# Performance work log

Measured on AMD Instinct MI355X. Metric: run time of the kernel, lower is better.

The kernel has to match this reference:

```python
import jax, jax.numpy as jnp
import numpy as np

WS = 7       # window size
SHIFT = 3    # shift size (ws//2)
NH = 16      # num heads
DIM = 512    # channels
HH = 112
WW = 112
HIDDEN = int(DIM * 4.0)
EPS = 1e-5


def _rel_index():
    # Swin relative position index, [N, N] ints into the bias table
    coords = np.stack(np.meshgrid(np.arange(WS), np.arange(WS), indexing='ij')).reshape(2, -1)
    rel = coords[:, :, None] - coords[:, None, :]
    rel = rel.transpose(1, 2, 0) + (WS - 1)
    rel[:, :, 0] *= 2 * WS - 1
    return rel.sum(-1)


def _attn_mask():
    # shifted-window mask on HH x WW (already multiples of WS) -> [nW, N, N] with 0 / -1e9
    img = np.zeros((HH, WW), np.int32)
    cnt = 0
    sl = (slice(0, -WS), slice(-WS, -SHIFT), slice(-SHIFT, None))
    for h in sl:
        for w in sl:
            img[h, w] = cnt
            cnt += 1
    win = img.reshape(HH // WS, WS, WW // WS, WS).transpose(0, 2, 1, 3).reshape(-1, WS * WS)
    diff = win[:, None, :] - win[:, :, None]
    return np.where(diff == 0, 0.0, -1e9).astype(np.float32)


def setup_inputs() -> dict:
    key = jax.random.key(0)
    ks = jax.random.split(key, 8)
    s = 0.02
    return {
        'x': jax.random.normal(ks[0], (DIM, HH, WW), jnp.float32),
        'norm1_w': jnp.ones((DIM,), jnp.float32),
        'norm1_b': jnp.zeros((DIM,), jnp.float32),
        'qkv_w': jax.random.normal(ks[1], (3 * DIM, DIM), jnp.float32) * s,
        'qkv_b': jnp.zeros((3 * DIM,), jnp.float32),
        'proj_w': jax.random.normal(ks[2], (DIM, DIM), jnp.float32) * s,
        'proj_b': jnp.zeros((DIM,), jnp.float32),
        'rpb_table': jax.random.normal(ks[3], ((2 * WS - 1) ** 2, NH), jnp.float32) * s,
        'norm2_w': jnp.ones((DIM,), jnp.float32),
        'norm2_b': jnp.zeros((DIM,), jnp.float32),
        'fc1_w': jax.random.normal(ks[4], (HIDDEN, DIM), jnp.float32) * s,
        'fc1_b': jnp.zeros((HIDDEN,), jnp.float32),
        'fc2_w': jax.random.normal(ks[5], (DIM, HIDDEN), jnp.float32) * s,
        'fc2_b': jnp.zeros((DIM,), jnp.float32),
    }


def _ln(x_hwc, w, b):
    m = x_hwc.mean(-1, keepdims=True)
    v = x_hwc.var(-1, keepdims=True)
    return (x_hwc - m) / jnp.sqrt(v + EPS) * w + b


def reference(x, norm1_w, norm1_b, qkv_w, qkv_b, proj_w, proj_b, rpb_table,
              norm2_w, norm2_b, fc1_w, fc1_b, fc2_w, fc2_b):
    C, H, W = x.shape
    ws = WS
    N = ws * ws
    hd = C // NH
    scale = 1.0 / np.sqrt(hd).astype(np.float32)

    x_hwc = jnp.moveaxis(x, 0, -1)                       # [H,W,C]
    xn = _ln(x_hwc, norm1_w, norm1_b)
    xs = jnp.roll(xn, (-SHIFT, -SHIFT), (0, 1))          # cyclic shift
    # window partition -> [nW, N, C]
    xw = xs.reshape(H // ws, ws, W // ws, ws, C).transpose(0, 2, 1, 3, 4).reshape(-1, N, C)

    qkv = xw @ qkv_w.T + qkv_b                            # [nW,N,3C]
    q, k, v = jnp.split(qkv, 3, -1)
    heads = lambda t: t.reshape(-1, N, NH, hd).transpose(0, 2, 1, 3)  # [nW,H,N,hd]
    q, k, v = heads(q), heads(k), heads(v)

    attn = jnp.einsum('whnd,whmd->whnm', q * scale, k)    # [nW,H,N,N]
    idx = jnp.asarray(_rel_index().reshape(-1))
    bias = rpb_table[idx].reshape(N, N, NH).transpose(2, 0, 1)  # [H,N,N]
    mask = jnp.asarray(_attn_mask())                       # [nW,N,N]
    attn = attn + bias[None] + mask[:, None]
    attn = jax.nn.softmax(attn, -1)

    out = jnp.einsum('whnm,whmd->whnd', attn, v).transpose(0, 2, 1, 3).reshape(-1, N, C)
    out = out @ proj_w.T + proj_b
    # window unpartition + reverse shift
    out = out.reshape(H // ws, W // ws, ws, ws, C).transpose(0, 2, 1, 3, 4).reshape(H, W, C)
    out = jnp.roll(out, (SHIFT, SHIFT), (0, 1))

    x1 = x_hwc + out                                       # residual (DropPath rate 0)
    x2 = _ln(x1, norm2_w, norm2_b)
    h = jax.nn.gelu(x2.reshape(-1, C) @ fc1_w.T + fc1_b)
    m = (h @ fc2_w.T + fc2_b).reshape(H, W, C)
    y = x1 + m
    return jnp.moveaxis(y, -1, 0)                          # back to [C,H,W]
```

## Files before the change

### kernel.cpp

```cpp
#include <hip/hip_runtime.h>

#define NPIX 12544
#define CDIM 512
#define QKVN 1536
#define HIDDEN 2048

typedef unsigned short u16;
typedef unsigned int u32;

typedef short bf16x8 __attribute__((ext_vector_type(8)));
typedef float f32x4 __attribute__((ext_vector_type(4)));

static __device__ __forceinline__ u16 f2bf(float f) {
  u32 u = __float_as_uint(f);
  return (u16)((u + 0x7fffu + ((u >> 16) & 1u)) >> 16);
}
static __device__ __forceinline__ u32 pack2(float a, float b) {
  return (u32)f2bf(a) | ((u32)f2bf(b) << 16);
}
static __device__ __forceinline__ u32 packtrunc2(float lo, float hi) {
  return __builtin_amdgcn_perm(__float_as_uint(hi), __float_as_uint(lo), 0x07060302u);
}
static __device__ __forceinline__ void async_ld16(const void* g, void* l) {
  __builtin_amdgcn_global_load_lds((__attribute__((address_space(1))) void*)g,
                                   (__attribute__((address_space(3))) void*)l, 16, 0, 0);
}

__global__ __launch_bounds__(256) void convert_weights(
    const float* __restrict__ qw, const float* __restrict__ pw,
    const float* __restrict__ w1, const float* __restrict__ w2,
    u16* __restrict__ Wq, u16* __restrict__ Wp, u16* __restrict__ W1o, u16* __restrict__ W2o) {
  const int b = blockIdx.x;
  const float* src; u16* dst; long off;
  if (b < 768)       { src = qw; dst = Wq;  off = (long)b * 1024; }
  else if (b < 1024) { src = pw; dst = Wp;  off = (long)(b - 768) * 1024; }
  else if (b < 2048) { src = w1; dst = W1o; off = (long)(b - 1024) * 1024; }
  else               { src = w2; dst = W2o; off = (long)(b - 2048) * 1024; }
  const long i = off / 4 + threadIdx.x;
  const float4 v = ((const float4*)src)[i];
  ushort4 u;
  u.x = f2bf(v.x); u.y = f2bf(v.y); u.z = f2bf(v.z); u.w = f2bf(v.w);
  ((ushort4*)dst)[i] = u;
}

__global__ __launch_bounds__(256) void ln1_partial(const float* __restrict__ x,
                                                   float* __restrict__ psum, float* __restrict__ pssq) {
  const int p = blockIdx.x * 256 + threadIdx.x;
  const int c0 = blockIdx.y * 32;
  float s = 0.f, ss = 0.f;
#pragma unroll
  for (int c = 0; c < 32; c++) {
    const float v = x[(long)(c0 + c) * NPIX + p];
    s += v; ss += v * v;
  }
  psum[blockIdx.y * NPIX + p] = s;
  pssq[blockIdx.y * NPIX + p] = ss;
}

__global__ __launch_bounds__(256) void ln1_stats(const float* __restrict__ psum, const float* __restrict__ pssq,
                                                 float* __restrict__ mean, float* __restrict__ rstd) {
  const int p = blockIdx.x * 256 + threadIdx.x;
  float s = 0.f, ss = 0.f;
#pragma unroll
  for (int ch = 0; ch < 16; ch++) { s += psum[ch * NPIX + p]; ss += pssq[ch * NPIX + p]; }
  const float m = s * (1.f / 512.f);
  const float v = ss * (1.f / 512.f) - m * m;
  mean[p] = m;
  rstd[p] = rsqrtf(v + 1e-5f);
}

__global__ __launch_bounds__(256) void ln1_shift_part(const float* __restrict__ x,
    const float* __restrict__ mean, const float* __restrict__ rstd,
    const float* __restrict__ gw, const float* __restrict__ gb, u16* __restrict__ xw) {
  __shared__ float tile[32][65];
  const int p0 = blockIdx.x * 64;
  const int c0 = blockIdx.y * 32;
  const int t = threadIdx.x;
  {
    const int pl = t & 63;
    const int cl0 = t >> 6;
#pragma unroll
    for (int r = 0; r < 8; r++) {
      const int cl = r * 4 + cl0;
      tile[cl][pl] = x[(long)(c0 + cl) * NPIX + p0 + pl];
    }
  }
  __syncthreads();
  const int cl = t & 31;
  const int g = t >> 5;
  const float wc = gw[c0 + cl];
  const float bc = gb[c0 + cl];
#pragma unroll
  for (int pass = 0; pass < 8; pass++) {
    const int pl = pass * 8 + g;
    const int p = p0 + pl;
    const int h = p / 112;
    const int w = p - h * 112;
    int hs = h + 109; if (hs >= 112) hs -= 112;
    int ws2 = w + 109; if (ws2 >= 112) ws2 -= 112;
    const int hq = hs / 7, wq = ws2 / 7;
    const int tok = (hq * 16 + wq) * 49 + (hs - hq * 7) * 7 + (ws2 - wq * 7);
    const float val = (tile[cl][pl] - mean[p]) * rstd[p] * wc + bc;
    xw[(long)tok * 512 + c0 + cl] = f2bf(val);
  }
}

template<bool OUT_BF16, bool DO_GELU, bool REMAP>
__global__ __launch_bounds__(256, 3) void gemm_bt(
    const u16* __restrict__ A, const u16* __restrict__ B,
    const float* __restrict__ bias, void* __restrict__ out,
    const int N, const int K) {
  __shared__ __align__(16) u16 Asm[128 * 32];
  __shared__ __align__(16) u16 Bsm[128 * 32];
  const int M0 = blockIdx.x << 7;
  const int N0 = blockIdx.y << 7;
  const int t = threadIdx.x;
  const int wave = t >> 6;
  const int lane = t & 63;
  const int l15 = lane & 15;
  const int quad = lane >> 4;
  const int wm = wave & 1;
  const int wn = wave >> 1;
  const int swz = (l15 >> 1) & 3;

  f32x4 acc[4][4] = {};

  for (int k0 = 0; k0 < K; k0 += 32) {
#pragma unroll
    for (int i = 0; i < 2; i++) {
      const int flatbase = i * 256 + wave * 64;
      const int FL = flatbase + lane;
      const int row = FL >> 2;
      const int chunk = (FL & 3) ^ ((row >> 1) & 3);
      async_ld16(A + (long)(M0 + row) * K + k0 + chunk * 8, &Asm[flatbase * 8]);
      async_ld16(B + (long)(N0 + row) * K + k0 + chunk * 8, &Bsm[flatbase * 8]);
    }
    __syncthreads();
    bf16x8 af[4], bfr[4];
#pragma unroll
    for (int im = 0; im < 4; im++)
      af[im] = *(const bf16x8*)&Asm[(wm * 64 + im * 16 + l15) * 32 + (quad ^ swz) * 8];
#pragma unroll
    for (int in = 0; in < 4; in++)
      bfr[in] = *(const bf16x8*)&Bsm[(wn * 64 + in * 16 + l15) * 32 + (quad ^ swz) * 8];
#pragma unroll
    for (int im = 0; im < 4; im++)
#pragma unroll
      for (int in = 0; in < 4; in++)
        acc[im][in] = __builtin_amdgcn_mfma_f32_16x16x32_bf16(bfr[in], af[im], acc[im][in], 0, 0, 0);
    __syncthreads();
  }

#pragma unroll
  for (int im = 0; im < 4; im++) {
    const int row = M0 + wm * 64 + im * 16 + l15;
    long orow = row;
    if (REMAP) {
      const int win = row / 49;
      const int nn = row - win * 49;
      const int nq = nn / 7;
      const int hs = (win >> 4) * 7 + nq;
      const int wsx = (win & 15) * 7 + (nn - nq * 7);
      int h = hs + 3; if (h >= 112) h -= 112;
      int w = wsx + 3; if (w >= 112) w -= 112;
      orow = h * 112 + w;
    }
#pragma unroll
    for (int in = 0; in < 4; in++) {
      const int col0 = N0 + wn * 64 + in * 16 + quad * 4;
      const float4 bv = *(const float4*)(bias + col0);
      float v[4];
#pragma unroll
      for (int r = 0; r < 4; r++) {
        float vv = acc[im][in][r] + ((const float*)&bv)[r];
        if (DO_GELU) {
          const float z2 = 1.5957691216f * (vv + 0.044715f * vv * vv * vv);
          vv = vv / (1.0f + __expf(-z2));
        }
        v[r] = vv;
      }
      if (OUT_BF16) {
        uint2 u;
        u.x = pack2(v[0], v[1]);
        u.y = pack2(v[2], v[3]);
        *(uint2*)((u16*)out + orow * (long)N + col0) = u;
      } else {
        float4 f; f.x = v[0]; f.y = v[1]; f.z = v[2]; f.w = v[3];
        *(float4*)((float*)out + orow * (long)N + col0) = f;
      }
    }
  }
}

__global__ __launch_bounds__(256) void build_biasT(const float* __restrict__ rpb, float* __restrict__ biasT) {
  const int cls = blockIdx.x >> 4;
  const int head = blockIdx.x & 15;
  for (int e = threadIdx.x; e < 4096; e += 256) {
    const int j = e >> 6;
    const int i = e & 63;
    float v;
    if (j >= 49) v = -1e9f;
    else if (i >= 49) v = 0.f;
    else {
      const int ri = i / 7, ci = i - (i / 7) * 7;
      const int rj = j / 7, cj = j - (j / 7) * 7;
      v = rpb[((ri - rj + 6) * 13 + (ci - cj + 6)) * 16 + head];
      const int lhi = (cls & 2) ? (ri < 4 ? 1 : 2) : 0;
      const int lwi = (cls & 1) ? (ci < 4 ? 1 : 2) : 0;
      const int lhj = (cls & 2) ? (rj < 4 ? 1 : 2) : 0;
      const int lwj = (cls & 1) ? (cj < 4 ? 1 : 2) : 0;
      if (lhi * 3 + lwi != lhj * 3 + lwj) v = -1e9f;
    }
    biasT[(long)blockIdx.x * 4096 + e] = v;
  }
}

__global__ __launch_bounds__(256, 3) void attn_mfma(
    const u16* __restrict__ qkv, const float* __restrict__ biasT, u16* __restrict__ out) {
  __shared__ __align__(16) u16 slds[24576];
  const int t = threadIdx.x;
  const int wave = t >> 6;
  const int lane = t & 63;
  const int l15 = lane & 15;
  const int quad = lane >> 4;
  const int win = blockIdx.x >> 2;
  const int head = (blockIdx.x & 3) * 4 + wave;
  const int cls = (((win >> 4) == 15) ? 2 : 0) | (((win & 15) == 15) ? 1 : 0);

  u16* Qb  = slds + wave * 6144;
  u16* Kb  = Qb + 2048;
  u16* Vtb = Qb + 4096;
  u16* Pb  = Qb;

  const int rrow = lane >> 2;
  const int chunk = (lane & 3) ^ ((lane >> 3) & 3);
  uint4 vv[4];
#pragma unroll
  for (int it = 0; it < 4; it++) {
    const int row = it * 16 + rrow;
    const int jc = row < 49 ? row : 48;
    const long gbase = (long)(win * 49 + jc) * 1536 + head * 32 + chunk * 8;
    async_ld16(qkv + gbase,       Qb + it * 512 + lane * 8);
    async_ld16(qkv + gbase + 512, Kb + it * 512 + lane * 8);
    vv[it] = *(const uint4*)(qkv + gbase + 1024);
  }
  __syncthreads();

#pragma unroll
  for (int it = 0; it < 4; it++) {
    const int row = it * 16 + rrow;
    const u32* w = (const u32*)&vv[it];
#pragma unroll
    for (int tt = 0; tt < 8; tt++) {
      const int d = chunk * 8 + tt;
      const u16 val = (tt & 1) ? (u16)(w[tt >> 1] >> 16) : (u16)(w[tt >> 1] & 0xffffu);
      Vtb[d * 64 + (row ^ (((d >> 2) & 3) << 4))] = val;
    }
  }

  const int fswz = (l15 >> 1) & 3;
  bf16x8 kfrag[4], qfrag[4];
#pragma unroll
  for (int jm = 0; jm < 4; jm++)
    kfrag[jm] = *(const bf16x8*)(Kb + (jm * 16 + l15) * 32 + (quad ^ fswz) * 8);
#pragma unroll
  for (int in = 0; in < 4; in++)
    qfrag[in] = *(const bf16x8*)(Qb + (in * 16 + l15) * 32 + (quad ^ fswz) * 8);
  f32x4 sacc[4][4] = {};
#pragma unroll
  for (int jm = 0; jm < 4; jm++)
#pragma unroll
    for (int in = 0; in < 4; in++)
      sacc[jm][in] = __builtin_amdgcn_mfma_f32_16x16x32_bf16(kfrag[jm], qfrag[in], sacc[jm][in], 0, 0, 0);

  const float* bT = biasT + (long)(cls * 16 + head) * 4096;
  const float sc = 0.17677669529663687f;
#pragma unroll
  for (int jm = 0; jm < 4; jm++) {
    const float* bp = bT + (jm * 16 + quad * 4) * 64 + l15;
#pragma unroll
    for (int in = 0; in < 4; in++)
#pragma unroll
      for (int r = 0; r < 4; r++)
        sacc[jm][in][r] = sacc[jm][in][r] * sc + bp[r * 64 + in * 16];
  }
  float linv[4];
#pragma unroll
  for (int in = 0; in < 4; in++) {
    float m = -1e30f;
#pragma unroll
    for (int jm = 0; jm < 4; jm++)
#pragma unroll
      for (int r = 0; r < 4; r++) m = fmaxf(m, sacc[jm][in][r]);
    m = fmaxf(m, __shfl_xor(m, 16));
    m = fmaxf(m, __shfl_xor(m, 32));
    float s = 0.f;
#pragma unroll
    for (int jm = 0; jm < 4; jm++)
#pragma unroll
      for (int r = 0; r < 4; r++) {
        const float e = __expf(sacc[jm][in][r] - m);
        sacc[jm][in][r] = e; s += e;
      }
    s += __shfl_xor(s, 16);
    s += __shfl_xor(s, 32);
    linv[in] = __builtin_amdgcn_rcpf(s);
  }

#pragma unroll
  for (int in = 0; in < 4; in++) {
    const int i = in * 16 + l15;
    const int rot = (l15 & 3) << 4;
#pragma unroll
    for (int jm = 0; jm < 4; jm++) {
      const u32 lo = packtrunc2(sacc[jm][in][0], sacc[jm][in][1]);
      const u32 hi = packtrunc2(sacc[jm][in][2], sacc[jm][in][3]);
      uint2 u; u.x = lo; u.y = hi;
      *(uint2*)(Pb + i * 64 + ((jm * 16 + quad * 4) ^ rot)) = u;
    }
  }

  f32x4 oacc[2][4] = {};
#pragma unroll
  for (int ks = 0; ks < 2; ks++) {
    bf16x8 vtf[2], pf[4];
#pragma unroll
    for (int dm = 0; dm < 2; dm++)
      vtf[dm] = *(const bf16x8*)(Vtb + (dm * 16 + l15) * 64 + ((ks * 32 + quad * 8) ^ ((l15 >> 2) << 4)));
#pragma unroll
    for (int in = 0; in < 4; in++)
      pf[in] = *(const bf16x8*)(Pb + (in * 16 + l15) * 64 + ((ks * 32 + quad * 8) ^ ((l15 & 3) << 4)));
#pragma unroll
    for (int dm = 0; dm < 2; dm++)
#pragma unroll
      for (int in = 0; in < 4; in++)
        oacc[dm][in] = __builtin_amdgcn_mfma_f32_16x16x32_bf16(vtf[dm], pf[in], oacc[dm][in], 0, 0, 0);
  }

#pragma unroll
  for (int in = 0; in < 4; in++) {
    const int i = in * 16 + l15;
    if (i < 49) {
      const float inv = linv[in];
      const long base = (long)(win * 49 + i) * 512 + head * 32 + quad * 4;
#pragma unroll
      for (int dm = 0; dm < 2; dm++) {
        const float v0 = oacc[dm][in][0] * inv, v1 = oacc[dm][in][1] * inv;
        const float v2 = oacc[dm][in][2] * inv, v3 = oacc[dm][in][3] * inv;
        uint2 u; u.x = packtrunc2(v0, v1); u.y = packtrunc2(v2, v3);
        *(uint2*)(out + base + dm * 16) = u;
      }
    }
  }
}

__global__ __launch_bounds__(256) void resid_kernel(const float* __restrict__ x,
    const float* __restrict__ proj, float* __restrict__ x1) {
  __shared__ float tile[32][65];
  const int p0 = blockIdx.x * 64;
  const int c0 = blockIdx.y * 32;
  const int t = threadIdx.x;
  {
    const int pl = t & 63;
    const int cl0 = t >> 6;
#pragma unroll
    for (int r = 0; r < 8; r++) {
      const int cl = r * 4 + cl0;
      tile[cl][pl] = x[(long)(c0 + cl) * NPIX + p0 + pl];
    }
  }
  __syncthreads();
  const int cl = t & 31;
  const int g = t >> 5;
#pragma unroll
  for (int pass = 0; pass < 8; pass++) {
    const int pl = pass * 8 + g;
    const long idx = (long)(p0 + pl) * 512 + c0 + cl;
    x1[idx] = tile[cl][pl] + proj[idx];
  }
}

__global__ __launch_bounds__(256) void ln2_apply(const float* __restrict__ x1,
    const float* __restrict__ gw, const float* __restrict__ gb, u16* __restrict__ x2) {
  const int wave = threadIdx.x >> 6;
  const int lane = threadIdx.x & 63;
  const int p = blockIdx.x * 4 + wave;
  const float4* row = (const float4*)(x1 + (long)p * 512);
  const float4 a = row[lane * 2];
  const float4 b = row[lane * 2 + 1];
  float s = a.x + a.y + a.z + a.w + b.x + b.y + b.z + b.w;
  float ss = a.x * a.x + a.y * a.y + a.z * a.z + a.w * a.w
           + b.x * b.x + b.y * b.y + b.z * b.z + b.w * b.w;
#pragma unroll
  for (int o = 32; o > 0; o >>= 1) { s += __shfl_xor(s, o); ss += __shfl_xor(ss, o); }
  const float m = s * (1.f / 512.f);
  const float var = ss * (1.f / 512.f) - m * m;
  const float rs = rsqrtf(var + 1e-5f);
  const float4 w0 = ((const float4*)gw)[lane * 2];
  const float4 w1 = ((const float4*)gw)[lane * 2 + 1];
  const float4 b0 = ((const float4*)gb)[lane * 2];
  const float4 b1 = ((const float4*)gb)[lane * 2 + 1];
  uint4 u;
  u.x = pack2((a.x - m) * rs * w0.x + b0.x, (a.y - m) * rs * w0.y + b0.y);
  u.y = pack2((a.z - m) * rs * w0.z + b0.z, (a.w - m) * rs * w0.w + b0.w);
  u.z = pack2((b.x - m) * rs * w1.x + b1.x, (b.y - m) * rs * w1.y + b1.y);
  u.w = pack2((b.z - m) * rs * w1.z + b1.z, (b.w - m) * rs * w1.w + b1.w);
  ((uint4*)(x2 + (long)p * 512))[lane] = u;
}

__global__ __launch_bounds__(256) void final_kernel(const float* __restrict__ x1,
    const float* __restrict__ mm, float* __restrict__ y) {
  __shared__ float tile[32][65];
  const int p0 = blockIdx.x * 64;
  const int c0 = blockIdx.y * 32;
  const int t = threadIdx.x;
  {
    const int cl = t & 31;
    const int g = t >> 5;
#pragma unroll
    for (int pass = 0; pass < 8; pass++) {
      const int pl = pass * 8 + g;
      const long idx = (long)(p0 + pl) * 512 + c0 + cl;
      tile[cl][pl] = x1[idx] + mm[idx];
    }
  }
  __syncthreads();
  const int pl = t & 63;
  const int cl0 = t >> 6;
#pragma unroll
  for (int r = 0; r < 8; r++) {
    const int cl = r * 4 + cl0;
    y[(long)(c0 + cl) * NPIX + p0 + pl] = tile[cl][pl];
  }
}

extern "C" void kernel_launch(void* const* d_in, const int* in_sizes, int n_in,
                              void* d_out, int out_size, void* d_ws, size_t ws_size,
                              hipStream_t stream) {
  (void)in_sizes; (void)n_in; (void)out_size; (void)ws_size;
  const float* x      = (const float*)d_in[0];
  const float* n1w    = (const float*)d_in[1];
  const float* n1b    = (const float*)d_in[2];
  const float* qkv_w  = (const float*)d_in[3];
  const float* qkv_b  = (const float*)d_in[4];
  const float* proj_w = (const float*)d_in[5];
  const float* proj_b = (const float*)d_in[6];
  const float* rpb    = (const float*)d_in[7];
  const float* n2w    = (const float*)d_in[8];
  const float* n2b    = (const float*)d_in[9];
  const float* fc1_w  = (const float*)d_in[10];
  const float* fc1_b  = (const float*)d_in[11];
  const float* fc2_w  = (const float*)d_in[12];
  const float* fc2_b  = (const float*)d_in[13];
  float* y = (float*)d_out;

  char* base = (char*)d_ws;
  size_t off = 0;
  auto alloc = [&](size_t b) { char* p = base + off; off += (b + 255) & ~(size_t)255; return p; };
  float* mean1 = (float*)alloc((size_t)NPIX * 4);
  float* rstd1 = (float*)alloc((size_t)NPIX * 4);
  float* psum  = (float*)alloc((size_t)16 * NPIX * 4);
  float* pssq  = (float*)alloc((size_t)16 * NPIX * 4);
  u16* Wq = (u16*)alloc((size_t)QKVN * CDIM * 2);
  u16* Wp = (u16*)alloc((size_t)CDIM * CDIM * 2);
  u16* W1 = (u16*)alloc((size_t)HIDDEN * CDIM * 2);
  u16* W2 = (u16*)alloc((size_t)CDIM * HIDDEN * 2);
  float* biasT = (float*)alloc((size_t)4 * 16 * 4096 * 4);
  u16* bufA = (u16*)alloc((size_t)NPIX * CDIM * 2);
  char* bufB = alloc((size_t)NPIX * QKVN * 2);
  float* x1 = (float*)alloc((size_t)NPIX * CDIM * 4);
  u16* hbuf = (u16*)alloc((size_t)NPIX * HIDDEN * 2);

  u16* xw      = bufA;
  u16* qkvbuf  = (u16*)bufB;
  u16* attnout = bufA;
  float* projout = (float*)bufB;
  u16* x2 = bufA;
  float* mbuf = (float*)bufB;

  convert_weights<<<3072, 256, 0, stream>>>(qkv_w, proj_w, fc1_w, fc2_w, Wq, Wp, W1, W2);
  build_biasT<<<64, 256, 0, stream>>>(rpb, biasT);

  ln1_partial<<<dim3(49, 16), 256, 0, stream>>>(x, psum, pssq);
  ln1_stats<<<49, 256, 0, stream>>>(psum, pssq, mean1, rstd1);
  ln1_shift_part<<<dim3(196, 16), 256, 0, stream>>>(x, mean1, rstd1, n1w, n1b, xw);

  gemm_bt<true, false, false><<<dim3(98, QKVN / 128), 256, 0, stream>>>(xw, Wq, qkv_b, qkvbuf, QKVN, CDIM);
  attn_mfma<<<1024, 256, 0, stream>>>(qkvbuf, biasT, attnout);
  gemm_bt<false, false, true><<<dim3(98, CDIM / 128), 256, 0, stream>>>(attnout, Wp, proj_b, projout, CDIM, CDIM);

  resid_kernel<<<dim3(196, 16), 256, 0, stream>>>(x, projout, x1);
  ln2_apply<<<NPIX / 4, 256, 0, stream>>>(x1, n2w, n2b, x2);

  gemm_bt<true, true, false><<<dim3(98, HIDDEN / 128), 256, 0, stream>>>(x2, W1, fc1_b, hbuf, HIDDEN, CDIM);
  gemm_bt<false, false, false><<<dim3(98, CDIM / 128), 256, 0, stream>>>(hbuf, W2, fc2_b, mbuf, CDIM, HIDDEN);

  final_kernel<<<dim3(196, 16), 256, 0, stream>>>(x1, mbuf, y);
}
```

Measured before the change: 331.5 us.

## Double GEMM K-tile to 64 and fuse residual plus transpose into fc2 epilogue

The GEMM K-step grows from 32 to 64 with an 8-way XOR swizzle, which halves the number of barrier pairs per tile and doubles the LDS footprint. The fc2 GEMM epilogue now adds the x1 residual and writes directly to the channel-major output, which removes the final transpose kernel and the intermediate fp32 mbuf round trip. The transposed stores are strided per element (stride NPIX), so the writes may be poorly coalesced. The larger LDS tile may also limit occupancy.

```diff
diff --git a/kernel.cpp b/kernel.cpp
--- a/kernel.cpp
+++ b/kernel.cpp
@@ -105,13 +105,13 @@
   }
 }
 
-template<bool OUT_BF16, bool DO_GELU, bool REMAP>
+template<bool OUT_BF16, bool DO_GELU, bool REMAP, bool FUSE_Y>
 __global__ __launch_bounds__(256, 3) void gemm_bt(
     const u16* __restrict__ A, const u16* __restrict__ B,
     const float* __restrict__ bias, void* __restrict__ out,
-    const int N, const int K) {
-  __shared__ __align__(16) u16 Asm[128 * 32];
-  __shared__ __align__(16) u16 Bsm[128 * 32];
+    const float* __restrict__ x1, const int N, const int K) {
+  __shared__ __align__(16) u16 Asm[128 * 64];
+  __shared__ __align__(16) u16 Bsm[128 * 64];
   const int M0 = blockIdx.x << 7;
   const int N0 = blockIdx.y << 7;
   const int t = threadIdx.x;
@@ -121,33 +121,36 @@
   const int quad = lane >> 4;
   const int wm = wave & 1;
   const int wn = wave >> 1;
-  const int swz = (l15 >> 1) & 3;
+  const int swz8 = l15 & 7;
 
   f32x4 acc[4][4] = {};
 
-  for (int k0 = 0; k0 < K; k0 += 32) {
-#pragma unroll
-    for (int i = 0; i < 2; i++) {
+  for (int k0 = 0; k0 < K; k0 += 64) {
+#pragma unroll
+    for (int i = 0; i < 4; i++) {
       const int flatbase = i * 256 + wave * 64;
       const int FL = flatbase + lane;
-      const int row = FL >> 2;
-      const int chunk = (FL & 3) ^ ((row >> 1) & 3);
-      async_ld16(A + (long)(M0 + row) * K + k0 + chunk * 8, &Asm[flatbase * 8]);
-      async_ld16(B + (long)(N0 + row) * K + k0 + chunk * 8, &Bsm[flatbase * 8]);
+      const int row = FL >> 3;
+      const int c = (FL & 7) ^ (row & 7);
+      async_ld16(A + (long)(M0 + row) * K + k0 + c * 8, Asm + flatbase * 8);
+      async_ld16(B + (long)(N0 + row) * K + k0 + c * 8, Bsm + flatbase * 8);
     }
     __syncthreads();
-    bf16x8 af[4], bfr[4];
-#pragma unroll
-    for (int im = 0; im < 4; im++)
-      af[im] = *(const bf16x8*)&Asm[(wm * 64 + im * 16 + l15) * 32 + (quad ^ swz) * 8];
-#pragma unroll
-    for (int in = 0; in < 4; in++)
-      bfr[in] = *(const bf16x8*)&Bsm[(wn * 64 + in * 16 + l15) * 32 + (quad ^ swz) * 8];
-#pragma unroll
-    for (int im = 0; im < 4; im++)
+#pragma unroll
+    for (int ks = 0; ks < 2; ks++) {
+      bf16x8 af[4], bfr[4];
+#pragma unroll
+      for (int im = 0; im < 4; im++)
+        af[im] = *(const bf16x8*)&Asm[(wm * 64 + im * 16 + l15) * 64 + ((ks * 4 + quad) ^ swz8) * 8];
 #pragma unroll
       for (int in = 0; in < 4; in++)
-        acc[im][in] = __builtin_amdgcn_mfma_f32_16x16x32_bf16(bfr[in], af[im], acc[im][in], 0, 0, 0);
+        bfr[in] = *(const bf16x8*)&Bsm[(wn * 64 + in * 16 + l15) * 64 + ((ks * 4 + quad) ^ swz8) * 8];
+#pragma unroll
+      for (int im = 0; im < 4; im++)
+#pragma unroll
+        for (int in = 0; in < 4; in++)
+          acc[im][in] = __builtin_amdgcn_mfma_f32_16x16x32_bf16(bfr[in], af[im], acc[im][in], 0, 0, 0);
+    }
     __syncthreads();
   }
 
@@ -170,23 +173,33 @@
       const int col0 = N0 + wn * 64 + in * 16 + quad * 4;
       const float4 bv = *(const float4*)(bias + col0);
       float v[4];
-#pragma unroll
-      for (int r = 0; r < 4; r++) {
-        float vv = acc[im][in][r] + ((const float*)&bv)[r];
-        if (DO_GELU) {
-          const float z2 = 1.5957691216f * (vv + 0.044715f * vv * vv * vv);
-          vv = vv / (1.0f + __expf(-z2));
+      if (FUSE_Y) {
+        const float4 xv = *(const float4*)(x1 + (long)row * CDIM + col0);
+#pragma unroll
+        for (int r = 0; r < 4; r++)
+          v[r] = acc[im][in][r] + ((const float*)&bv)[r] + ((const float*)&xv)[r];
+#pragma unroll
+        for (int r = 0; r < 4; r++)
+          ((float*)out)[(long)(col0 + r) * NPIX + row] = v[r];
+      } else {
+#pragma unroll
+        for (int r = 0; r < 4; r++) {
+          float vv = acc[im][in][r] + ((const float*)&bv)[r];
+          if (DO_GELU) {
+            const float z2 = 1.5957691216f * (vv + 0.044715f * vv * vv * vv);
+            vv = vv / (1.0f + __expf(-z2));
+          }
+          v[r] = vv;
         }
-        v[r] = vv;
-      }
-      if (OUT_BF16) {
-        uint2 u;
-        u.x = pack2(v[0], v[1]);
-        u.y = pack2(v[2], v[3]);
-        *(uint2*)((u16*)out + orow * (long)N + col0) = u;
-      } else {
-        float4 f; f.x = v[0]; f.y = v[1]; f.z = v[2]; f.w = v[3];
-        *(float4*)((float*)out + orow * (long)N + col0) = f;
+        if (OUT_BF16) {
+          uint2 u;
+          u.x = pack2(v[0], v[1]);
+          u.y = pack2(v[2], v[3]);
+          *(uint2*)((u16*)out + orow * (long)N + col0) = u;
+        } else {
+          float4 f; f.x = v[0]; f.y = v[1]; f.z = v[2]; f.w = v[3];
+          *(float4*)((float*)out + orow * (long)N + col0) = f;
+        }
       }
     }
   }
@@ -406,32 +419,6 @@
   u.z = pack2((b.x - m) * rs * w1.x + b1.x, (b.y - m) * rs * w1.y + b1.y);
   u.w = pack2((b.z - m) * rs * w1.z + b1.z, (b.w - m) * rs * w1.w + b1.w);
   ((uint4*)(x2 + (long)p * 512))[lane] = u;
-}
-
-__global__ __launch_bounds__(256) void final_kernel(const float* __restrict__ x1,
-    const float* __restrict__ mm, float* __restrict__ y) {
-  __shared__ float tile[32][65];
-  const int p0 = blockIdx.x * 64;
-  const int c0 = blockIdx.y * 32;
-  const int t = threadIdx.x;
-  {
-    const int cl = t & 31;
-    const int g = t >> 5;
-#pragma unroll
-    for (int pass = 0; pass < 8; pass++) {
-      const int pl = pass * 8 + g;
-      const long idx = (long)(p0 + pl) * 512 + c0 + cl;
-      tile[cl][pl] = x1[idx] + mm[idx];
-    }
-  }
-  __syncthreads();
-  const int pl = t & 63;
-  const int cl0 = t >> 6;
-#pragma unroll
-  for (int r = 0; r < 8; r++) {
-    const int cl = r * 4 + cl0;
-    y[(long)(c0 + cl) * NPIX + p0 + pl] = tile[cl][pl];
-  }
 }
 
 extern "C" void kernel_launch(void* const* d_in, const int* in_sizes, int n_in,
@@ -476,7 +463,6 @@
   u16* attnout = bufA;
   float* projout = (float*)bufB;
   u16* x2 = bufA;
-  float* mbuf = (float*)bufB;
 
   convert_weights<<<3072, 256, 0, stream>>>(qkv_w, proj_w, fc1_w, fc2_w, Wq, Wp, W1, W2);
   build_biasT<<<64, 256, 0, stream>>>(rpb, biasT);
@@ -485,15 +471,13 @@
   ln1_stats<<<49, 256, 0, stream>>>(psum, pssq, mean1, rstd1);
   ln1_shift_part<<<dim3(196, 16), 256, 0, stream>>>(x, mean1, rstd1, n1w, n1b, xw);
 
-  gemm_bt<true, false, false><<<dim3(98, QKVN / 128), 256, 0, stream>>>(xw, Wq, qkv_b, qkvbuf, QKVN, CDIM);
+  gemm_bt<true, false, false, false><<<dim3(98, QKVN / 128), 256, 0, stream>>>(xw, Wq, qkv_b, qkvbuf, nullptr, QKVN, CDIM);
   attn_mfma<<<1024, 256, 0, stream>>>(qkvbuf, biasT, attnout);
-  gemm_bt<false, false, true><<<dim3(98, CDIM / 128), 256, 0, stream>>>(attnout, Wp, proj_b, projout, CDIM, CDIM);
+  gemm_bt<false, false, true, false><<<dim3(98, CDIM / 128), 256, 0, stream>>>(attnout, Wp, proj_b, projout, nullptr, CDIM, CDIM);
 
   resid_kernel<<<dim3(196, 16), 256, 0, stream>>>(x, projout, x1);
   ln2_apply<<<NPIX / 4, 256, 0, stream>>>(x1, n2w, n2b, x2);
 
-  gemm_bt<true, true, false><<<dim3(98, HIDDEN / 128), 256, 0, stream>>>(x2, W1, fc1_b, hbuf, HIDDEN, CDIM);
-  gemm_bt<false, false, false><<<dim3(98, CDIM / 128), 256, 0, stream>>>(hbuf, W2, fc2_b, mbuf, CDIM, HIDDEN);
-
-  final_kernel<<<dim3(196, 16), 256, 0, stream>>>(x1, mbuf, y);
-}
+  gemm_bt<true, true, false, false><<<dim3(98, HIDDEN / 128), 256, 0, stream>>>(x2, W1, fc1_b, hbuf, nullptr, HIDDEN, CDIM);
+  gemm_bt<false, false, false, true><<<dim3(98, CDIM / 128), 256, 0, stream>>>(hbuf, W2, fc2_b, y, x1, CDIM, HIDDEN);
+}
```

Result: faster. 306.6 us (-7.5%).
